# Kernel tuning notes

Hardware: AMD Instinct MI355X
Metric: run time of the kernel (lower is better)

## Reference

```python
import jax, jax.numpy as jnp
import numpy as np

EPS_MASK = 1e-9   # module fills masked scores with eps, NOT -inf
LN_EPS = 1e-5

def _layer_norm(x, g, b):
    mu = jnp.mean(x, axis=-1, keepdims=True)
    var = jnp.mean(jnp.square(x - mu), axis=-1, keepdims=True)
    return (x - mu) * jax.lax.rsqrt(var + LN_EPS) * g + b

def _mha(q_in, k_in, v_in, wq, bq, wk, bk, wv, bv, wo, bo, mask, nhead):
    B, Sq, D = q_in.shape
    dk = D // nhead
    def proj(x, w, b):
        y = x @ w + b                                   # [B,S,D]
        return y.reshape(B, -1, nhead, dk).transpose(0, 2, 1, 3)  # [B,h,S,dk]
    q, k, v = proj(q_in, wq, bq), proj(k_in, wk, bk), proj(v_in, wv, bv)
    scores = jnp.einsum('bhqd,bhkd->bhqk', q, k) / np.sqrt(dk).astype(q.dtype)
    if mask is not None:
        scores = jnp.where(mask[:, None, :, :] == 0, jnp.asarray(EPS_MASK, scores.dtype), scores)
    p = jax.nn.softmax(scores, axis=-1)                 # dropout = identity (eval)
    x = jnp.einsum('bhqk,bhkd->bhqd', p, v)
    x = x.transpose(0, 2, 1, 3).reshape(B, Sq, D)
    return x @ wo + bo

def _forward_post(tgt, memory, tgt_pos, memory_pos, tgt_mask, memory_mask, p):
    nhead = 8
    # self-attention (q=k=tgt+pos, v=tgt)
    q = tgt + tgt_pos
    sa = _mha(q, q, tgt, p['sa_wq'], p['sa_bq'], p['sa_wk'], p['sa_bk'],
              p['sa_wv'], p['sa_bv'], p['sa_wo'], p['sa_bo'], tgt_mask, nhead)
    tgt = _layer_norm(tgt + sa, p['ln1_g'], p['ln1_b'])
    # cross-attention (q=tgt+tgt_pos, k=memory+memory_pos, v=memory)
    mq = tgt + tgt_pos
    mk = memory + memory_pos
    ca = _mha(mq, mk, memory, p['ca_wq'], p['ca_bq'], p['ca_wk'], p['ca_bk'],
              p['ca_wv'], p['ca_bv'], p['ca_wo'], p['ca_bo'], memory_mask, nhead)
    tgt = _layer_norm(tgt + ca, p['ln2_g'], p['ln2_b'])
    # FFN
    h = jax.nn.relu(tgt @ p['mlp_w1'] + p['mlp_b1'])
    ff = h @ p['mlp_w2'] + p['mlp_b2']
    return _layer_norm(tgt + ff, p['ln3_g'], p['ln3_b'])

def setup_inputs() -> dict:
    key = jax.random.key(0)
    B, S, M, D, H = 4, 1024, 1024, 512, 2048
    ks = iter(jax.random.split(key, 40))
    d = {
        'tgt': jax.random.normal(next(ks), (B, S, D), jnp.float32),
        'memory': jax.random.normal(next(ks), (B, M, D), jnp.float32),
        'tgt_pos': jax.random.normal(next(ks), (B, S, D), jnp.float32),
        'memory_pos': jax.random.normal(next(ks), (B, M, D), jnp.float32),
        'tgt_mask': jax.random.randint(next(ks), (B, S, S), 0, 2, jnp.int32),
        'memory_mask': jax.random.randint(next(ks), (B, S, M), 0, 2, jnp.int32),
    }
    for pre in ('sa', 'ca'):
        for nm in ('q', 'k', 'v', 'o'):
            d[f'{pre}_w{nm}'] = jax.random.normal(next(ks), (D, D), jnp.float32) * 0.02
            d[f'{pre}_b{nm}'] = jnp.zeros((D,), jnp.float32)
    for i in (1, 2, 3):
        d[f'ln{i}_g'] = jnp.ones((D,), jnp.float32)
        d[f'ln{i}_b'] = jnp.zeros((D,), jnp.float32)
    d['mlp_w1'] = jax.random.normal(next(ks), (D, H), jnp.float32) * 0.02
    d['mlp_b1'] = jnp.zeros((H,), jnp.float32)
    d['mlp_w2'] = jax.random.normal(next(ks), (H, D), jnp.float32) * 0.02
    d['mlp_b2'] = jnp.zeros((D,), jnp.float32)
    return d

def reference(tgt, memory, tgt_pos, memory_pos, tgt_mask, memory_mask,
              sa_wq, sa_bq, sa_wk, sa_bk, sa_wv, sa_bv, sa_wo, sa_bo,
              ca_wq, ca_bq, ca_wk, ca_bk, ca_wv, ca_bv, ca_wo, ca_bo,
              ln1_g, ln1_b, ln2_g, ln2_b, ln3_g, ln3_b,
              mlp_w1, mlp_b1, mlp_w2, mlp_b2):
    p = dict(sa_wq=sa_wq, sa_bq=sa_bq, sa_wk=sa_wk, sa_bk=sa_bk, sa_wv=sa_wv,
             sa_bv=sa_bv, sa_wo=sa_wo, sa_bo=sa_bo, ca_wq=ca_wq, ca_bq=ca_bq,
             ca_wk=ca_wk, ca_bk=ca_bk, ca_wv=ca_wv, ca_bv=ca_bv, ca_wo=ca_wo,
             ca_bo=ca_bo, ln1_g=ln1_g, ln1_b=ln1_b, ln2_g=ln2_g, ln2_b=ln2_b,
             ln3_g=ln3_g, ln3_b=ln3_b, mlp_w1=mlp_w1, mlp_b1=mlp_b1,
             mlp_w2=mlp_w2, mlp_b2=mlp_b2)
    return _forward_post(tgt, memory, tgt_pos, memory_pos, tgt_mask, memory_mask, p)
```

## Files before the change

### kernel.cpp

```cpp
#include <hip/hip_runtime.h>
#include <stdint.h>

typedef unsigned int u32;
typedef unsigned long long u64;
typedef unsigned short u16;
typedef __attribute__((ext_vector_type(8))) __bf16 bf16x8;
typedef __attribute__((ext_vector_type(4))) float f32x4;

#define DEV __device__ __forceinline__

DEV u16 f2bf(float f) {
    u32 x = __builtin_bit_cast(u32, f);
    u32 r = (x + 0x7FFFu + ((x >> 16) & 1u)) >> 16;
    return (u16)r;
}

DEV float bf2f(u16 x) {
    u32 u = (u32)x << 16;
    return __builtin_bit_cast(float, u);
}

DEV void unp8(uint4 u, float* f) {
    f[0] = bf2f((u16)u.x); f[1] = bf2f((u16)(u.x >> 16));
    f[2] = bf2f((u16)u.y); f[3] = bf2f((u16)(u.y >> 16));
    f[4] = bf2f((u16)u.z); f[5] = bf2f((u16)(u.z >> 16));
    f[6] = bf2f((u16)u.w); f[7] = bf2f((u16)(u.w >> 16));
}

DEV bf16x8 ldg8(const u16* p) {
    return __builtin_bit_cast(bf16x8, *(const uint4*)p);
}

DEV u32 pk2(float a, float b) {
    return (u32)f2bf(a) | ((u32)f2bf(b) << 16);
}

DEV void g2l16(const u16* g, u16* l) {
    __builtin_amdgcn_global_load_lds(
        (const __attribute__((address_space(1))) u32*)g,
        (__attribute__((address_space(3))) u32*)l, 16, 0, 0);
}

DEV f32x4 mfma16(bf16x8 a, bf16x8 b, f32x4 c) {
    return __builtin_amdgcn_mfma_f32_16x16x32_bf16(a, b, c, 0, 0, 0);
}

struct ProArgs {
    const float* w[10];
    u16* wtbase;
    const float4 *tgt, *tpos, *mem, *mpos;
    ushort4 *qin, *tgtb, *memb, *mkb, *tposb;
    const int4 *m1, *m2;
    u32 *o1, *o2;
};
__global__ __launch_bounds__(256) void prologue_kernel(ProArgs a) {
    const int bx = blockIdx.x, t = threadIdx.x;
    if (bx < 10240) {
        int z = bx >> 10, bxx = bx & 1023;
        int Kd = (z == 9) ? 2048 : 512;
        int Nd = (z == 8) ? 2048 : 512;
        size_t off = (z < 8) ? (size_t)z * 262144
                             : (z == 8 ? (size_t)2097152 : (size_t)3145728);
        u16* out = a.wtbase + off;
        int nx = Nd / 32;
        int txile = bxx % nx, tyile = bxx / nx;
        if (tyile >= Kd / 32) return;
        const float* w = a.w[z];
        __shared__ float tl[32][33];
        int tx = t & 31, ty = t >> 5;
#pragma unroll
        for (int j = 0; j < 4; ++j)
            tl[ty + j * 8][tx] = w[(size_t)(tyile * 32 + ty + j * 8) * Nd + txile * 32 + tx];
        __syncthreads();
#pragma unroll
        for (int j = 0; j < 4; ++j)
            out[(size_t)(txile * 32 + ty + j * 8) * Kd + tyile * 32 + tx] = f2bf(tl[tx][ty + j * 8]);
    } else if (bx < 12288) {
        int i = (bx - 10240) * 256 + t;
        float4 tt = a.tgt[i], p = a.tpos[i], m = a.mem[i], mp = a.mpos[i];
        a.qin[i]  = make_ushort4(f2bf(tt.x + p.x), f2bf(tt.y + p.y), f2bf(tt.z + p.z), f2bf(tt.w + p.w));
        a.tgtb[i] = make_ushort4(f2bf(tt.x), f2bf(tt.y), f2bf(tt.z), f2bf(tt.w));
        a.memb[i] = make_ushort4(f2bf(m.x), f2bf(m.y), f2bf(m.z), f2bf(m.w));
        a.mkb[i]  = make_ushort4(f2bf(m.x + mp.x), f2bf(m.y + mp.y), f2bf(m.z + mp.z), f2bf(m.w + mp.w));
        a.tposb[i]= make_ushort4(f2bf(p.x), f2bf(p.y), f2bf(p.z), f2bf(p.w));
    } else {
        int i = (bx - 12288) * 256 + t;
        const int n8 = 524288;
        bool first = i < n8;
        int idx = first ? i : i - n8;
        const int4* src = first ? a.m1 : a.m2;
        int4 x = src[idx * 2], y = src[idx * 2 + 1];
        u32 by = (u32)(x.x != 0) | ((u32)(x.y != 0) << 1) | ((u32)(x.z != 0) << 2) |
                 ((u32)(x.w != 0) << 3) | ((u32)(y.x != 0) << 4) | ((u32)(y.y != 0) << 5) |
                 ((u32)(y.z != 0) << 6) | ((u32)(y.w != 0) << 7);
        u32 w = by | (__shfl_down(by, 1) << 8) | (__shfl_down(by, 2) << 16) |
                (__shfl_down(by, 3) << 24);
        if ((t & 3) == 0) (first ? a.o1 : a.o2)[idx >> 2] = w;
    }
}

struct GemmSet {
    const u16* A; const u16* W; const float* bias; void* out;
    float oscale; int epi; int k0; int klen;
};
struct GemmArgs5 { GemmSet s[5]; };

template <int BM, int BN>
__global__ __launch_bounds__(256) void gemm_kernel(GemmArgs5 args, int M, int N, int Kd) {
    constexpr int MF = BM / 32, NF = BN / 32;
    const GemmSet gs = args.s[blockIdx.z];
    const u16* __restrict__ A = gs.A;
    const u16* __restrict__ W = gs.W;
    const int t = threadIdx.x;
    const int lane = t & 63;
    const int g = lane >> 4, r16 = lane & 15;
    const int wave = t >> 6;
    const int wm = wave >> 1, wn = wave & 1;
    const int nwg = gridDim.x * gridDim.y;
    const int fid = blockIdx.y * gridDim.x + blockIdx.x;
    const int qq = nwg >> 3;
    const int lid = (fid & 7) * qq + (fid >> 3);
    const int m0 = (lid / gridDim.x) * BM, n0 = (lid % gridDim.x) * BN;

    __shared__ __align__(16) u16 As[BM * 64];
    __shared__ __align__(16) u16 Bs[BN * 64];

    f32x4 acc[MF][NF];
#pragma unroll
    for (int m = 0; m < MF; ++m)
#pragma unroll
        for (int n = 0; n < NF; ++n) acc[m][n] = f32x4{0.f, 0.f, 0.f, 0.f};

    const int kend = gs.k0 + gs.klen;
    for (int kk = gs.k0; kk < kend; kk += 64) {
        __syncthreads();
#pragma unroll
        for (int i = 0; i < BM / 32; ++i) {
            int cid = t + i * 256, row = cid >> 3, c = cid & 7;
            g2l16(A + (size_t)(m0 + row) * Kd + kk + ((c ^ (row & 7)) << 3), &As[cid << 3]);
        }
#pragma unroll
        for (int i = 0; i < BN / 32; ++i) {
            int cid = t + i * 256, row = cid >> 3, c = cid & 7;
            g2l16(W + (size_t)(n0 + row) * Kd + kk + ((c ^ (row & 7)) << 3), &Bs[cid << 3]);
        }
        __syncthreads();
#pragma unroll
        for (int ks = 0; ks < 2; ++ks) {
            bf16x8 af[MF], bfr[NF];
#pragma unroll
            for (int m = 0; m < MF; ++m) {
                int row = wm * (MF * 16) + m * 16 + r16;
                af[m] = *(const bf16x8*)&As[(row << 6) + (((ks * 4 + g) ^ (row & 7)) << 3)];
            }
#pragma unroll
            for (int n = 0; n < NF; ++n) {
                int row = wn * (NF * 16) + n * 16 + r16;
                bfr[n] = *(const bf16x8*)&Bs[(row << 6) + (((ks * 4 + g) ^ (row & 7)) << 3)];
            }
#pragma unroll
            for (int m = 0; m < MF; ++m)
#pragma unroll
                for (int n = 0; n < NF; ++n)
                    acc[m][n] = mfma16(af[m], bfr[n], acc[m][n]);
        }
    }
    const int epi = gs.epi;
#pragma unroll
    for (int m = 0; m < MF; ++m) {
        int row0 = m0 + wm * (MF * 16) + m * 16 + g * 4;
#pragma unroll
        for (int n = 0; n < NF; ++n) {
            int col = n0 + wn * (NF * 16) + n * 16 + r16;
            float bv = gs.bias ? gs.bias[col] : 0.f;
            float v[4];
#pragma unroll
            for (int r = 0; r < 4; ++r) v[r] = (acc[m][n][r] + bv) * gs.oscale;
            if (epi == 1) {
#pragma unroll
                for (int r = 0; r < 4; ++r) v[r] = fmaxf(v[r], 0.f);
            }
            if (epi == 3) {
                int bb = row0 >> 10, s = row0 & 1023;
                u16* o = (u16*)gs.out +
                         ((size_t)(bb * 8 + (col >> 6)) * 64 + (col & 63)) * 1024 + s;
                *(ushort4*)o = make_ushort4(f2bf(v[0]), f2bf(v[1]), f2bf(v[2]), f2bf(v[3]));
            } else {
                u16* o = (u16*)gs.out;
#pragma unroll
                for (int r = 0; r < 4; ++r) o[(size_t)(row0 + r) * N + col] = f2bf(v[r]);
            }
        }
    }
}

__global__ __launch_bounds__(512) void attn_part_kernel(
    const u16* __restrict__ Q, const u16* __restrict__ K,
    const u16* __restrict__ VT, const u32* __restrict__ mb,
    u16* __restrict__ OP, float2* __restrict__ ML, int Lq, int Lk) {
    const int t = threadIdx.x, lane = t & 63, wave = t >> 6;
    const int g = lane >> 4, r16 = lane & 15;
    const int h = blockIdx.y;
    const int b = blockIdx.z >> 1, p = blockIdx.z & 1;
    const int bh = b * 8 + h;
    const int q0 = blockIdx.x * 128 + wave * 16;
    const int kc0 = p * (Lk >> 1);
    const int NCH = (Lk >> 1) >> 5;

    __shared__ __align__(16) u16 Ks[2][32][64];
    __shared__ __align__(16) u16 Vs[2][64][32];
    __shared__ __align__(16) u16 Pl[8][16][40];

    const size_t qrow = (size_t)b * Lq + q0 + r16;
    const u16* qp = Q + qrow * 512 + h * 64 + g * 8;
    bf16x8 qb0 = ldg8(qp), qb1 = ldg8(qp + 32);
    const u32* mrow = mb + qrow * (Lk >> 5);

    const int sid = t & 255;
    const bool isK = t < 256;
    const int srow = sid >> 3, sc = sid & 7;
    const int vd = sid >> 2, vc = sid & 3;
    const u16* sg = isK
        ? K + (size_t)b * Lk * 512 + h * 64 + (size_t)srow * 512 + ((sc ^ (srow & 7)) << 3)
        : VT + ((size_t)bh * 64 + vd) * Lk + (vc << 3);
    u16* const sl = (isK ? &Ks[0][0][0] : &Vs[0][0][0]) + sid * 8;
    const size_t sstride = isK ? 512 : 1;

    f32x4 acc[4];
#pragma unroll
    for (int dt = 0; dt < 4; ++dt) acc[dt] = f32x4{0.f, 0.f, 0.f, 0.f};
    float mrun = -INFINITY, lrun = 0.f;
    const f32x4 zf = {0.f, 0.f, 0.f, 0.f};

    g2l16(sg + (size_t)kc0 * sstride, sl);
    __syncthreads();

    for (int c = 0; c < NCH; ++c) {
        const int buf = c & 1, nbuf = buf ^ 1;
        const int kc = kc0 + c * 32;
        if (c + 1 < NCH)
            g2l16(sg + (size_t)(kc + 32) * sstride, sl + nbuf * 2048);
        const u16* kb = &Ks[buf][0][0];
        const u16* vb = &Vs[buf][0][0];
        const int r1 = 16 + r16;
        bf16x8 k00 = *(const bf16x8*)(kb + r16 * 64 + ((g ^ (r16 & 7)) << 3));
        bf16x8 k01 = *(const bf16x8*)(kb + r16 * 64 + (((4 + g) ^ (r16 & 7)) << 3));
        bf16x8 k10 = *(const bf16x8*)(kb + r1 * 64 + ((g ^ (r16 & 7)) << 3));
        bf16x8 k11 = *(const bf16x8*)(kb + r1 * 64 + (((4 + g) ^ (r16 & 7)) << 3));
        f32x4 s0 = mfma16(k00, qb0, zf); s0 = mfma16(k01, qb1, s0);
        f32x4 s1 = mfma16(k10, qb0, zf); s1 = mfma16(k11, qb1, s1);

        u32 mw = mrow[kc >> 5];
        float sv[8];
#pragma unroll
        for (int r = 0; r < 4; ++r) {
            sv[r]     = ((mw >> (g * 4 + r)) & 1) ? s0[r] : 1e-9f;
            sv[4 + r] = ((mw >> (16 + g * 4 + r)) & 1) ? s1[r] : 1e-9f;
        }
        float tm = fmaxf(fmaxf(fmaxf(sv[0], sv[1]), fmaxf(sv[2], sv[3])),
                         fmaxf(fmaxf(sv[4], sv[5]), fmaxf(sv[6], sv[7])));
        tm = fmaxf(tm, __shfl_xor(tm, 16));
        tm = fmaxf(tm, __shfl_xor(tm, 32));
        if (!__all(tm <= mrun + 8.f)) {
            float mn = fmaxf(mrun, tm);
            float alpha = __expf(mrun - mn);
            mrun = mn;
            lrun *= alpha;
#pragma unroll
            for (int r = 0; r < 4; ++r) {
                float ar = __shfl(alpha, g * 4 + r);
#pragma unroll
                for (int dt = 0; dt < 4; ++dt) acc[dt][r] *= ar;
            }
        }
        float ts = 0.f;
#pragma unroll
        for (int j = 0; j < 8; ++j) { sv[j] = __expf(sv[j] - mrun); ts += sv[j]; }
        ts += __shfl_xor(ts, 16);
        ts += __shfl_xor(ts, 32);
        lrun += ts;

        uint2 u0; u0.x = pk2(sv[0], sv[1]); u0.y = pk2(sv[2], sv[3]);
        uint2 u1; u1.x = pk2(sv[4], sv[5]); u1.y = pk2(sv[6], sv[7]);
        *(uint2*)&Pl[wave][r16][g * 4] = u0;
        *(uint2*)&Pl[wave][r16][16 + g * 4] = u1;
        bf16x8 pf = *(const bf16x8*)&Pl[wave][r16][g * 8];
#pragma unroll
        for (int dt = 0; dt < 4; ++dt) {
            bf16x8 vf = *(const bf16x8*)(vb + (dt * 16 + r16) * 32 + g * 8);
            acc[dt] = mfma16(pf, vf, acc[dt]);
        }
        __syncthreads();
    }

    if (lane < 16)
        ML[(size_t)p * 32768 + (size_t)bh * 1024 + q0 + lane] = make_float2(mrun, lrun);
    const size_t obase = (size_t)p * 2097152 + ((size_t)bh * 1024 + q0) * 64;
#pragma unroll
    for (int dt = 0; dt < 4; ++dt)
#pragma unroll
        for (int r = 0; r < 4; ++r)
            OP[obase + (size_t)(g * 4 + r) * 64 + dt * 16 + r16] = f2bf(acc[dt][r]);
}

__global__ __launch_bounds__(256) void attn_combine_kernel(
    const u16* __restrict__ OP, const float2* __restrict__ ML, u16* __restrict__ O) {
    int gid = blockIdx.x * 256 + threadIdx.x;
    int row = gid >> 3, seg = gid & 7;
    size_t idx = (size_t)row * 64 + seg * 8;
    float2 ml0 = ML[row], ml1 = ML[32768 + row];
    float M = fmaxf(ml0.x, ml1.x);
    float w0 = __expf(ml0.x - M), w1 = __expf(ml1.x - M);
    float rden = 1.f / (ml0.y * w0 + ml1.y * w1);
    w0 *= rden; w1 *= rden;
    float a[8], b[8];
    unp8(*(const uint4*)(OP + idx), a);
    unp8(*(const uint4*)(OP + 2097152 + idx), b);
    int bh = row >> 10, q = row & 1023;
    int bb = bh >> 3, h = bh & 7;
    u16* o = O + ((size_t)(bb * 1024 + q)) * 512 + h * 64 + seg * 8;
    uint4 r;
    r.x = pk2(a[0] * w0 + b[0] * w1, a[1] * w0 + b[1] * w1);
    r.y = pk2(a[2] * w0 + b[2] * w1, a[3] * w0 + b[3] * w1);
    r.z = pk2(a[4] * w0 + b[4] * w1, a[5] * w0 + b[5] * w1);
    r.w = pk2(a[6] * w0 + b[6] * w1, a[7] * w0 + b[7] * w1);
    *(uint4*)o = r;
}

template <int MODE>
__global__ __launch_bounds__(256) void ln_kernel(
    const u16* __restrict__ a, const u16* __restrict__ b1, const u16* __restrict__ b2,
    const float* __restrict__ gam, const float* __restrict__ bet,
    const u16* __restrict__ pos,
    u16* __restrict__ yb, u16* __restrict__ qb, float* __restrict__ yf) {
    const int lane = threadIdx.x & 63;
    const int row = blockIdx.x * 4 + (threadIdx.x >> 6);
    const size_t base = (size_t)row * 512 + lane * 8;
    float av[8], bv[8], cv[8];
    unp8(*(const uint4*)(a + base), av);
    unp8(*(const uint4*)(b1 + base), bv);
    unp8(*(const uint4*)(b2 + base), cv);
    float x[8];
#pragma unroll
    for (int j = 0; j < 8; ++j) x[j] = av[j] + bv[j] + cv[j];
    float s1 = 0.f, s2 = 0.f;
#pragma unroll
    for (int j = 0; j < 8; ++j) { s1 += x[j]; s2 += x[j] * x[j]; }
#pragma unroll
    for (int d = 1; d < 64; d <<= 1) { s1 += __shfl_xor(s1, d); s2 += __shfl_xor(s2, d); }
    float mean = s1 * (1.f / 512.f);
    float var = s2 * (1.f / 512.f) - mean * mean;
    float rs = rsqrtf(var + 1e-5f);
    float4 gv0 = ((const float4*)(gam + lane * 8))[0];
    float4 gv1 = ((const float4*)(gam + lane * 8))[1];
    float4 be0 = ((const float4*)(bet + lane * 8))[0];
    float4 be1 = ((const float4*)(bet + lane * 8))[1];
    float gg[8] = {gv0.x, gv0.y, gv0.z, gv0.w, gv1.x, gv1.y, gv1.z, gv1.w};
    float bb[8] = {be0.x, be0.y, be0.z, be0.w, be1.x, be1.y, be1.z, be1.w};
    float y[8];
#pragma unroll
    for (int j = 0; j < 8; ++j) y[j] = (x[j] - mean) * rs * gg[j] + bb[j];
    if (MODE == 2) {
        ((float4*)(yf + base))[0] = make_float4(y[0], y[1], y[2], y[3]);
        ((float4*)(yf + base))[1] = make_float4(y[4], y[5], y[6], y[7]);
        return;
    }
    uint4 r;
    r.x = pk2(y[0], y[1]); r.y = pk2(y[2], y[3]);
    r.z = pk2(y[4], y[5]); r.w = pk2(y[6], y[7]);
    *(uint4*)(yb + base) = r;
    if (MODE == 0) {
        float pv[8];
        unp8(*(const uint4*)(pos + base), pv);
        uint4 q;
        q.x = pk2(y[0] + pv[0], y[1] + pv[1]);
        q.y = pk2(y[2] + pv[2], y[3] + pv[3]);
        q.z = pk2(y[4] + pv[4], y[5] + pv[5]);
        q.w = pk2(y[6] + pv[6], y[7] + pv[7]);
        *(uint4*)(qb + base) = q;
    }
}

extern "C" void kernel_launch(void* const* d_in, const int* in_sizes, int n_in,
                              void* d_out, int out_size, void* d_ws, size_t ws_size,
                              hipStream_t stream) {
    (void)in_sizes; (void)n_in; (void)out_size; (void)ws_size;
    const float* tgt      = (const float*)d_in[0];
    const float* memory   = (const float*)d_in[1];
    const float* tgt_pos  = (const float*)d_in[2];
    const float* mem_pos  = (const float*)d_in[3];
    const int*   tgt_mask = (const int*)d_in[4];
    const int*   mem_mask = (const int*)d_in[5];
    const float* sa_b[4] = {(const float*)d_in[7], (const float*)d_in[9],
                            (const float*)d_in[11], (const float*)d_in[13]};
    const float* ca_b[4] = {(const float*)d_in[15], (const float*)d_in[17],
                            (const float*)d_in[19], (const float*)d_in[21]};
    const float* ln1_g = (const float*)d_in[22]; const float* ln1_b = (const float*)d_in[23];
    const float* ln2_g = (const float*)d_in[24]; const float* ln2_b = (const float*)d_in[25];
    const float* ln3_g = (const float*)d_in[26]; const float* ln3_b = (const float*)d_in[27];
    const float* mlp_b1 = (const float*)d_in[29];
    const float* mlp_b2 = (const float*)d_in[31];

    const size_t MiB = 1024 * 1024;
    char* ws = (char*)d_ws;
    u16*  WT  = (u16*)(ws + 0);
    u32*  MBS = (u32*)(ws + 8 * MiB);
    u32*  MBC = (u32*)(ws + 8 * MiB + 512 * 1024);
    u16*  QIN = (u16*)(ws + 9 * MiB);
    u16*  TGTB= (u16*)(ws + 13 * MiB);
    u16*  MEMB= (u16*)(ws + 17 * MiB);
    u16*  MKB = (u16*)(ws + 21 * MiB);
    u16*  QM  = (u16*)(ws + 25 * MiB);
    u16*  KMS = (u16*)(ws + 29 * MiB);
    u16*  KMC = (u16*)(ws + 33 * MiB);
    u16*  VTS = (u16*)(ws + 37 * MiB);
    u16*  VTC = (u16*)(ws + 41 * MiB);
    u16*  ATNB= (u16*)(ws + 45 * MiB);
    u16*  P1B = (u16*)(ws + 49 * MiB);
    u16*  P2B = (u16*)(ws + 69 * MiB);
    u16*  X1B = (u16*)(ws + 53 * MiB);
    u16*  MQB = (u16*)(ws + 57 * MiB);
    u16*  X2B = (u16*)(ws + 61 * MiB);
    u16*  TPB = (u16*)(ws + 65 * MiB);
    u16*  FFH = (u16*)(ws + 9 * MiB);
    u16*  OPB = (u16*)(ws + 96 * MiB);
    float2* MLB = (float2*)(ws + 120 * MiB);

    u16* wt[10];
    for (int z = 0; z < 8; ++z) wt[z] = WT + (size_t)z * 262144;
    wt[8] = WT + 2097152;
    wt[9] = WT + 3145728;

    ProArgs pa;
    pa.w[0] = (const float*)d_in[6];  pa.w[1] = (const float*)d_in[8];
    pa.w[2] = (const float*)d_in[10]; pa.w[3] = (const float*)d_in[12];
    pa.w[4] = (const float*)d_in[14]; pa.w[5] = (const float*)d_in[16];
    pa.w[6] = (const float*)d_in[18]; pa.w[7] = (const float*)d_in[20];
    pa.w[8] = (const float*)d_in[28]; pa.w[9] = (const float*)d_in[30];
    pa.wtbase = WT;
    pa.tgt = (const float4*)tgt; pa.tpos = (const float4*)tgt_pos;
    pa.mem = (const float4*)memory; pa.mpos = (const float4*)mem_pos;
    pa.qin = (ushort4*)QIN; pa.tgtb = (ushort4*)TGTB;
    pa.memb = (ushort4*)MEMB; pa.mkb = (ushort4*)MKB;
    pa.tposb = (ushort4*)TPB;
    pa.m1 = (const int4*)tgt_mask; pa.m2 = (const int4*)mem_mask;
    pa.o1 = MBS; pa.o2 = MBC;
    prologue_kernel<<<16384, 256, 0, stream>>>(pa);

    GemmArgs5 ga;
    ga.s[0] = {QIN,  wt[0], sa_b[0], QM,  0.125f, 0, 0, 512};
    ga.s[1] = {QIN,  wt[1], sa_b[1], KMS, 1.f,    0, 0, 512};
    ga.s[2] = {TGTB, wt[2], sa_b[2], VTS, 1.f,    3, 0, 512};
    ga.s[3] = {MKB,  wt[5], ca_b[1], KMC, 1.f,    0, 0, 512};
    ga.s[4] = {MEMB, wt[6], ca_b[2], VTC, 1.f,    3, 0, 512};
    gemm_kernel<128, 64><<<dim3(8, 32, 5), 256, 0, stream>>>(ga, 4096, 512, 512);
    attn_part_kernel<<<dim3(8, 8, 8), 512, 0, stream>>>(QM, KMS, VTS, MBS, OPB, MLB, 1024, 1024);
    attn_combine_kernel<<<1024, 256, 0, stream>>>(OPB, MLB, ATNB);
    ga.s[0] = {ATNB, wt[3], sa_b[3], P1B, 1.f, 0, 0,   256};
    ga.s[1] = {ATNB, wt[3], nullptr, P2B, 1.f, 0, 256, 256};
    ga.s[2] = ga.s[0]; ga.s[3] = ga.s[0]; ga.s[4] = ga.s[0];
    gemm_kernel<64, 64><<<dim3(8, 64, 2), 256, 0, stream>>>(ga, 4096, 512, 512);
    ln_kernel<0><<<1024, 256, 0, stream>>>(TGTB, P1B, P2B, ln1_g, ln1_b, TPB, X1B, MQB, nullptr);

    ga.s[0] = {MQB, wt[4], ca_b[0], QM, 0.125f, 0, 0, 512};
    ga.s[1] = ga.s[0]; ga.s[2] = ga.s[0]; ga.s[3] = ga.s[0]; ga.s[4] = ga.s[0];
    gemm_kernel<64, 64><<<dim3(8, 64, 1), 256, 0, stream>>>(ga, 4096, 512, 512);
    attn_part_kernel<<<dim3(8, 8, 8), 512, 0, stream>>>(QM, KMC, VTC, MBC, OPB, MLB, 1024, 1024);
    attn_combine_kernel<<<1024, 256, 0, stream>>>(OPB, MLB, ATNB);
    ga.s[0] = {ATNB, wt[7], ca_b[3], P1B, 1.f, 0, 0,   256};
    ga.s[1] = {ATNB, wt[7], nullptr, P2B, 1.f, 0, 256, 256};
    ga.s[2] = ga.s[0]; ga.s[3] = ga.s[0]; ga.s[4] = ga.s[0];
    gemm_kernel<64, 64><<<dim3(8, 64, 2), 256, 0, stream>>>(ga, 4096, 512, 512);
    ln_kernel<1><<<1024, 256, 0, stream>>>(X1B, P1B, P2B, ln2_g, ln2_b, nullptr, X2B, nullptr, nullptr);

    ga.s[0] = {X2B, wt[8], mlp_b1, FFH, 1.f, 1, 0, 512};
    ga.s[1] = ga.s[0]; ga.s[2] = ga.s[0]; ga.s[3] = ga.s[0]; ga.s[4] = ga.s[0];
    gemm_kernel<128, 64><<<dim3(32, 32, 1), 256, 0, stream>>>(ga, 4096, 2048, 512);
    ga.s[0] = {FFH, wt[9], mlp_b2, P1B, 1.f, 0, 0,    1024};
    ga.s[1] = {FFH, wt[9], nullptr, P2B, 1.f, 0, 1024, 1024};
    ga.s[2] = ga.s[0]; ga.s[3] = ga.s[0]; ga.s[4] = ga.s[0];
    gemm_kernel<64, 64><<<dim3(8, 64, 2), 256, 0, stream>>>(ga, 4096, 512, 2048);
    ln_kernel<2><<<1024, 256, 0, stream>>>(X2B, P1B, P2B, ln3_g, ln3_b, nullptr,
                                           nullptr, nullptr, (float*)d_out);
}
```

Baseline: 169.3 us.

## Double attention key chunk to 64 with swizzled V tile and fixed lengths

The split-K attention kernel now processes 64 keys per chunk instead of 32, so there are half as many chunks, barriers and softmax rescale checks per block. The V tile moves to a 64x64 XOR-swizzled shared layout, and each thread issues two async global-to-LDS loads per stage. Sequence lengths become compile-time constants with a fully unrolled loop, and launch bounds now request 4 waves per SIMD. In exchange, LDS use doubles and the larger unrolled body raises register pressure, which could limit occupancy.

```diff
diff --git a/kernel.cpp b/kernel.cpp
--- a/kernel.cpp
+++ b/kernel.cpp
@@ -194,10 +194,11 @@
     }
 }
 
-__global__ __launch_bounds__(512) void attn_part_kernel(
+__global__ __launch_bounds__(512, 4) void attn_part_kernel(
     const u16* __restrict__ Q, const u16* __restrict__ K,
     const u16* __restrict__ VT, const u32* __restrict__ mb,
-    u16* __restrict__ OP, float2* __restrict__ ML, int Lq, int Lk) {
+    u16* __restrict__ OP, float2* __restrict__ ML) {
+    constexpr int Lq = 1024, Lk = 1024, NCH = 8;
     const int t = threadIdx.x, lane = t & 63, wave = t >> 6;
     const int g = lane >> 4, r16 = lane & 15;
     const int h = blockIdx.y;
@@ -205,11 +206,10 @@
     const int bh = b * 8 + h;
     const int q0 = blockIdx.x * 128 + wave * 16;
     const int kc0 = p * (Lk >> 1);
-    const int NCH = (Lk >> 1) >> 5;
-
-    __shared__ __align__(16) u16 Ks[2][32][64];
-    __shared__ __align__(16) u16 Vs[2][64][32];
-    __shared__ __align__(16) u16 Pl[8][16][40];
+
+    __shared__ __align__(16) u16 Ks[2][64][64];
+    __shared__ __align__(16) u16 Vs[2][64][64];
+    __shared__ __align__(16) u16 Pl[8][16][72];
 
     const size_t qrow = (size_t)b * Lq + q0 + r16;
     const u16* qp = Q + qrow * 512 + h * 64 + g * 8;
@@ -218,13 +218,23 @@
 
     const int sid = t & 255;
     const bool isK = t < 256;
-    const int srow = sid >> 3, sc = sid & 7;
-    const int vd = sid >> 2, vc = sid & 3;
-    const u16* sg = isK
-        ? K + (size_t)b * Lk * 512 + h * 64 + (size_t)srow * 512 + ((sc ^ (srow & 7)) << 3)
-        : VT + ((size_t)bh * 64 + vd) * Lk + (vc << 3);
-    u16* const sl = (isK ? &Ks[0][0][0] : &Vs[0][0][0]) + sid * 8;
-    const size_t sstride = isK ? 512 : 1;
+    const int s1 = sid, s2 = sid + 256;
+    const int r1 = s1 >> 3, c1 = s1 & 7;
+    const int r2 = s2 >> 3, c2 = s2 & 7;
+    const u16 *sgA, *sgB;
+    if (isK) {
+        const u16* kbase = K + (size_t)b * Lk * 512 + h * 64;
+        sgA = kbase + (size_t)(kc0 + r1) * 512 + ((c1 ^ (r1 & 7)) << 3);
+        sgB = kbase + (size_t)(kc0 + r2) * 512 + ((c2 ^ (r2 & 7)) << 3);
+    } else {
+        const u16* vbase = VT + (size_t)bh * 64 * Lk + kc0;
+        sgA = vbase + (size_t)r1 * Lk + ((c1 ^ (r1 & 7)) << 3);
+        sgB = vbase + (size_t)r2 * Lk + ((c2 ^ (r2 & 7)) << 3);
+    }
+    const size_t adv = isK ? (size_t)64 * 512 : 64;
+    u16* const base = isK ? &Ks[0][0][0] : &Vs[0][0][0];
+    u16* const slA = base + s1 * 8;
+    u16* const slB = base + s2 * 8;
 
     f32x4 acc[4];
 #pragma unroll
@@ -232,33 +242,46 @@
     float mrun = -INFINITY, lrun = 0.f;
     const f32x4 zf = {0.f, 0.f, 0.f, 0.f};
 
-    g2l16(sg + (size_t)kc0 * sstride, sl);
+    g2l16(sgA, slA);
+    g2l16(sgB, slB);
     __syncthreads();
 
+#pragma unroll
     for (int c = 0; c < NCH; ++c) {
         const int buf = c & 1, nbuf = buf ^ 1;
-        const int kc = kc0 + c * 32;
-        if (c + 1 < NCH)
-            g2l16(sg + (size_t)(kc + 32) * sstride, sl + nbuf * 2048);
+        const int kc = kc0 + c * 64;
+        if (c + 1 < NCH) {
+            g2l16(sgA + (size_t)(c + 1) * adv, slA + nbuf * 4096);
+            g2l16(sgB + (size_t)(c + 1) * adv, slB + nbuf * 4096);
+        }
         const u16* kb = &Ks[buf][0][0];
         const u16* vb = &Vs[buf][0][0];
-        const int r1 = 16 + r16;
-        bf16x8 k00 = *(const bf16x8*)(kb + r16 * 64 + ((g ^ (r16 & 7)) << 3));
-        bf16x8 k01 = *(const bf16x8*)(kb + r16 * 64 + (((4 + g) ^ (r16 & 7)) << 3));
-        bf16x8 k10 = *(const bf16x8*)(kb + r1 * 64 + ((g ^ (r16 & 7)) << 3));
-        bf16x8 k11 = *(const bf16x8*)(kb + r1 * 64 + (((4 + g) ^ (r16 & 7)) << 3));
-        f32x4 s0 = mfma16(k00, qb0, zf); s0 = mfma16(k01, qb1, s0);
-        f32x4 s1 = mfma16(k10, qb0, zf); s1 = mfma16(k11, qb1, s1);
-
-        u32 mw = mrow[kc >> 5];
-        float sv[8];
-#pragma unroll
-        for (int r = 0; r < 4; ++r) {
-            sv[r]     = ((mw >> (g * 4 + r)) & 1) ? s0[r] : 1e-9f;
-            sv[4 + r] = ((mw >> (16 + g * 4 + r)) & 1) ? s1[r] : 1e-9f;
+        f32x4 s[4];
+#pragma unroll
+        for (int j = 0; j < 4; ++j) {
+            int row = j * 16 + r16;
+            bf16x8 ka0 = *(const bf16x8*)(kb + row * 64 + ((g ^ (row & 7)) << 3));
+            bf16x8 ka1 = *(const bf16x8*)(kb + row * 64 + (((4 + g) ^ (row & 7)) << 3));
+            s[j] = mfma16(ka0, qb0, zf);
+            s[j] = mfma16(ka1, qb1, s[j]);
+        }
+        u32 mw0 = mrow[kc >> 5], mw1 = mrow[(kc >> 5) + 1];
+        float sv[16];
+#pragma unroll
+        for (int j = 0; j < 4; ++j) {
+            u32 w = (j < 2) ? mw0 : mw1;
+            int bbase = (16 * j) & 31;
+#pragma unroll
+            for (int r = 0; r < 4; ++r) {
+                int bit = bbase + g * 4 + r;
+                sv[4 * j + r] = ((w >> bit) & 1) ? s[j][r] : 1e-9f;
+            }
         }
         float tm = fmaxf(fmaxf(fmaxf(sv[0], sv[1]), fmaxf(sv[2], sv[3])),
                          fmaxf(fmaxf(sv[4], sv[5]), fmaxf(sv[6], sv[7])));
+        float tm2 = fmaxf(fmaxf(fmaxf(sv[8], sv[9]), fmaxf(sv[10], sv[11])),
+                          fmaxf(fmaxf(sv[12], sv[13]), fmaxf(sv[14], sv[15])));
+        tm = fmaxf(tm, tm2);
         tm = fmaxf(tm, __shfl_xor(tm, 16));
         tm = fmaxf(tm, __shfl_xor(tm, 32));
         if (!__all(tm <= mrun + 8.f)) {
@@ -275,20 +298,27 @@
         }
         float ts = 0.f;
 #pragma unroll
-        for (int j = 0; j < 8; ++j) { sv[j] = __expf(sv[j] - mrun); ts += sv[j]; }
+        for (int j = 0; j < 16; ++j) { sv[j] = __expf(sv[j] - mrun); ts += sv[j]; }
         ts += __shfl_xor(ts, 16);
         ts += __shfl_xor(ts, 32);
         lrun += ts;
 
-        uint2 u0; u0.x = pk2(sv[0], sv[1]); u0.y = pk2(sv[2], sv[3]);
-        uint2 u1; u1.x = pk2(sv[4], sv[5]); u1.y = pk2(sv[6], sv[7]);
-        *(uint2*)&Pl[wave][r16][g * 4] = u0;
-        *(uint2*)&Pl[wave][r16][16 + g * 4] = u1;
-        bf16x8 pf = *(const bf16x8*)&Pl[wave][r16][g * 8];
+#pragma unroll
+        for (int j = 0; j < 4; ++j) {
+            uint2 u;
+            u.x = pk2(sv[4 * j], sv[4 * j + 1]);
+            u.y = pk2(sv[4 * j + 2], sv[4 * j + 3]);
+            *(uint2*)&Pl[wave][r16][16 * j + g * 4] = u;
+        }
+        bf16x8 pf0 = *(const bf16x8*)&Pl[wave][r16][g * 8];
+        bf16x8 pf1 = *(const bf16x8*)&Pl[wave][r16][32 + g * 8];
 #pragma unroll
         for (int dt = 0; dt < 4; ++dt) {
-            bf16x8 vf = *(const bf16x8*)(vb + (dt * 16 + r16) * 32 + g * 8);
-            acc[dt] = mfma16(pf, vf, acc[dt]);
+            int row = dt * 16 + r16;
+            bf16x8 vf0 = *(const bf16x8*)(vb + row * 64 + ((g ^ (row & 7)) << 3));
+            bf16x8 vf1 = *(const bf16x8*)(vb + row * 64 + (((4 + g) ^ (row & 7)) << 3));
+            acc[dt] = mfma16(pf0, vf0, acc[dt]);
+            acc[dt] = mfma16(pf1, vf1, acc[dt]);
         }
         __syncthreads();
     }
@@ -417,11 +447,11 @@
     u16*  VTC = (u16*)(ws + 41 * MiB);
     u16*  ATNB= (u16*)(ws + 45 * MiB);
     u16*  P1B = (u16*)(ws + 49 * MiB);
-    u16*  P2B = (u16*)(ws + 69 * MiB);
     u16*  X1B = (u16*)(ws + 53 * MiB);
     u16*  MQB = (u16*)(ws + 57 * MiB);
     u16*  X2B = (u16*)(ws + 61 * MiB);
     u16*  TPB = (u16*)(ws + 65 * MiB);
+    u16*  P2B = (u16*)(ws + 69 * MiB);
     u16*  FFH = (u16*)(ws + 9 * MiB);
     u16*  OPB = (u16*)(ws + 96 * MiB);
     float2* MLB = (float2*)(ws + 120 * MiB);
@@ -454,7 +484,7 @@
     ga.s[3] = {MKB,  wt[5], ca_b[1], KMC, 1.f,    0, 0, 512};
     ga.s[4] = {MEMB, wt[6], ca_b[2], VTC, 1.f,    3, 0, 512};
     gemm_kernel<128, 64><<<dim3(8, 32, 5), 256, 0, stream>>>(ga, 4096, 512, 512);
-    attn_part_kernel<<<dim3(8, 8, 8), 512, 0, stream>>>(QM, KMS, VTS, MBS, OPB, MLB, 1024, 1024);
+    attn_part_kernel<<<dim3(8, 8, 8), 512, 0, stream>>>(QM, KMS, VTS, MBS, OPB, MLB);
     attn_combine_kernel<<<1024, 256, 0, stream>>>(OPB, MLB, ATNB);
     ga.s[0] = {ATNB, wt[3], sa_b[3], P1B, 1.f, 0, 0,   256};
     ga.s[1] = {ATNB, wt[3], nullptr, P2B, 1.f, 0, 256, 256};
@@ -465,7 +495,7 @@
     ga.s[0] = {MQB, wt[4], ca_b[0], QM, 0.125f, 0, 0, 512};
     ga.s[1] = ga.s[0]; ga.s[2] = ga.s[0]; ga.s[3] = ga.s[0]; ga.s[4] = ga.s[0];
     gemm_kernel<64, 64><<<dim3(8, 64, 1), 256, 0, stream>>>(ga, 4096, 512, 512);
-    attn_part_kernel<<<dim3(8, 8, 8), 512, 0, stream>>>(QM, KMC, VTC, MBC, OPB, MLB, 1024, 1024);
+    attn_part_kernel<<<dim3(8, 8, 8), 512, 0, stream>>>(QM, KMC, VTC, MBC, OPB, MLB);
     attn_combine_kernel<<<1024, 256, 0, stream>>>(OPB, MLB, ATNB);
     ga.s[0] = {ATNB, wt[7], ca_b[3], P1B, 1.f, 0, 0,   256};
     ga.s[1] = {ATNB, wt[7], nullptr, P2B, 1.f, 0, 256, 256};
```

After: 161.9 us. 4.4% less time.
